# Kernel optimization log

Measured on AMD Instinct MI355X. Metric: run time of the kernel, lower is better.

The kernel has to match this reference:

```python
import jax, jax.numpy as jnp
import numpy as np

INPUT_DIM = 1024
ATTN_DIM = 512
N1 = 4096
N2 = 4096


def setup_inputs() -> dict:
    key = jax.random.key(0)
    ks = jax.random.split(key, 10)
    s_in = 1.0 / np.sqrt(INPUT_DIM)   # torch Linear default init scale
    s_at = 1.0 / np.sqrt(ATTN_DIM)
    return {
        "input1": jax.random.normal(ks[0], (N1, INPUT_DIM), jnp.float32),
        "input2": jax.random.normal(ks[1], (N2, INPUT_DIM), jnp.float32),
        "Wq": jax.random.uniform(ks[2], (INPUT_DIM, ATTN_DIM), jnp.float32, -s_in, s_in),
        "bq": jax.random.uniform(ks[3], (ATTN_DIM,), jnp.float32, -s_in, s_in),
        "Wk": jax.random.uniform(ks[4], (INPUT_DIM, ATTN_DIM), jnp.float32, -s_in, s_in),
        "bk": jax.random.uniform(ks[5], (ATTN_DIM,), jnp.float32, -s_in, s_in),
        "Wv": jax.random.uniform(ks[6], (INPUT_DIM, ATTN_DIM), jnp.float32, -s_in, s_in),
        "bv": jax.random.uniform(ks[7], (ATTN_DIM,), jnp.float32, -s_in, s_in),
        "Wo": jax.random.uniform(ks[8], (ATTN_DIM, INPUT_DIM), jnp.float32, -s_at, s_at),
        "bo": jax.random.uniform(ks[9], (INPUT_DIM,), jnp.float32, -s_at, s_at),
    }


def reference(input1, input2, Wq, bq, Wk, bk, Wv, bv, Wo, bo):
    # shared projections for both inputs
    q1 = input1 @ Wq + bq            # [N1, A]
    q2 = input2 @ Wq + bq            # [N2, A]
    k1 = input1 @ Wk + bk
    k2 = input2 @ Wk + bk
    v1 = input1 @ Wv + bv
    v2 = input2 @ Wv + bv
    # cross attention 1: input1 queries attend to input2 keys/values
    attn1 = jax.nn.softmax(q1 @ k2.T, axis=-1)   # [N1, N2]
    attn2 = jax.nn.softmax(q2 @ k1.T, axis=-1)   # [N2, N1]
    out1 = (attn1 @ v2) @ Wo + bo                # [N1, input_dim]
    out2 = (attn2 @ v1) @ Wo + bo                # [N2, input_dim]
    return (out1, out2)
```

## Files before the change

### kernel.cpp

```cpp
#include <hip/hip_runtime.h>

typedef __bf16 bf16;
typedef _Float16 f16;
typedef __bf16 bf16x8 __attribute__((ext_vector_type(8)));
typedef _Float16 f16x8 __attribute__((ext_vector_type(8)));
typedef _Float16 f16x4 __attribute__((ext_vector_type(4)));
typedef float f32x4 __attribute__((ext_vector_type(4)));
typedef unsigned int u32x4 __attribute__((ext_vector_type(4)));

#define NROWS 4096
#define DIN 1024
#define DA 512
#define NCHUNK 64

template <typename T> struct V8;
template <> struct V8<f16> { using type = f16x8; };
template <> struct V8<bf16> { using type = bf16x8; };

__device__ __forceinline__ f32x4 mfma16(f16x8 a, f16x8 b, f32x4 c) {
  return __builtin_amdgcn_mfma_f32_16x16x32_f16(a, b, c, 0, 0, 0);
}
__device__ __forceinline__ f32x4 mfma16(bf16x8 a, bf16x8 b, f32x4 c) {
  return __builtin_amdgcn_mfma_f32_16x16x32_bf16(a, b, c, 0, 0, 0);
}

__device__ __forceinline__ void gload_lds16(const void* g, void* l) {
  __builtin_amdgcn_global_load_lds((const __attribute__((address_space(1))) void*)g,
                                   (__attribute__((address_space(3))) void*)l, 16, 0, 0);
}

template <int N> __device__ __forceinline__ void vmcnt_wait() {
  if constexpr (N == 0) asm volatile("s_waitcnt vmcnt(0)" ::: "memory");
  else if constexpr (N == 1) asm volatile("s_waitcnt vmcnt(1)" ::: "memory");
  else if constexpr (N == 2) asm volatile("s_waitcnt vmcnt(2)" ::: "memory");
  else if constexpr (N == 3) asm volatile("s_waitcnt vmcnt(3)" ::: "memory");
  else if constexpr (N == 4) asm volatile("s_waitcnt vmcnt(4)" ::: "memory");
  else if constexpr (N == 5) asm volatile("s_waitcnt vmcnt(5)" ::: "memory");
  else if constexpr (N == 6) asm volatile("s_waitcnt vmcnt(6)" ::: "memory");
  else if constexpr (N == 8) asm volatile("s_waitcnt vmcnt(8)" ::: "memory");
  else static_assert(N == 0, "unsupported vmcnt");
}


__global__ void cast_kernel(const float* __restrict__ s1, const float* __restrict__ s2,
                            f16* __restrict__ d1, f16* __restrict__ d2, int n) {
  const float* s = blockIdx.z ? s2 : s1;
  f16* d = blockIdx.z ? d2 : d1;
  int i = (blockIdx.x * blockDim.x + threadIdx.x) * 4;
  if (i < n) {
    float4 v = *(const float4*)(s + i);
    f16x4 o;
    o[0] = (f16)v.x; o[1] = (f16)v.y; o[2] = (f16)v.z; o[3] = (f16)v.w;
    *(f16x4*)(d + i) = o;
  }
}

__global__ void transpose_f32(const float* __restrict__ w0, const float* __restrict__ w1,
                              const float* __restrict__ w2, f16* __restrict__ dst,
                              size_t dstride, int rows, int cols) {
  const float* s = blockIdx.z == 0 ? w0 : (blockIdx.z == 1 ? w1 : w2);
  f16* d = dst + (size_t)blockIdx.z * dstride;
  __shared__ float tile[32][33];
  int bc = blockIdx.x * 32, br = blockIdx.y * 32;
  int tx = threadIdx.x, ty = threadIdx.y;
  for (int i = ty; i < 32; i += 8)
    tile[i][tx] = s[(size_t)(br + i) * cols + bc + tx];
  __syncthreads();
  for (int i = ty; i < 32; i += 8)
    d[(size_t)(bc + i) * rows + br + tx] = (f16)tile[tx][i];
}

__global__ void rowsum_reduce(const float* __restrict__ prsP, float* __restrict__ prsT) {
  int i = blockIdx.x * 256 + threadIdx.x;
  int z = i >> 12, row = i & 4095;
  const float* p = prsP + (size_t)z * NCHUNK * NROWS + row;
  float s = 0.f;
#pragma unroll
  for (int j = 0; j < NCHUNK; ++j) s += p[(size_t)j * NROWS];
  prsT[i] = s;
}

__global__ void merge_kernel(const f16* __restrict__ pO, f16* __restrict__ mid) {
  const size_t QS = (size_t)NROWS * DA;
  size_t e = ((size_t)blockIdx.x * blockDim.x + threadIdx.x) * 8;
  int z = (int)(e / QS);
  size_t rem = e - (size_t)z * QS;
  f16x8 a = *(const f16x8*)(pO + (size_t)z * QS + rem);
  f16x8 b = *(const f16x8*)(pO + (size_t)(2 + z) * QS + rem);
  f16x8 o;
#pragma unroll
  for (int j = 0; j < 8; ++j) o[j] = (f16)((float)a[j] + (float)b[j]);
  *(f16x8*)(mid + (size_t)z * QS + rem) = o;
}


template <typename TIN>
struct G8Args {
  const TIN* A[6];
  const TIN* B[6];
  const float* bias[6];
  void* C[6];
  float* rsO[6];
  int k0[6];
  int storebf[6];
  int lda, ldb, ldc, aK;
};

template <typename TIN, int EPI, int BN, int NT, int BK = 64, int MINW = 1, int PH = 4>
__global__ __launch_bounds__(512, MINW) void g8(G8Args<TIN> args) {
  using vec8 = typename V8<TIN>::type;
  constexpr int NFR = BN / 64;
  constexpr int FPP = 8 / PH;
  constexpr int KK = BK / 32;
  constexpr int RB = BK * 2;
  constexpr int CPR = RB / 16;
  constexpr int SWM = CPR - 1;
  constexpr int SFT = (CPR == 4) ? 1 : 0;
  constexpr int ABUF = 256 * RB;
  constexpr int BBUF = BN * RB;
  constexpr int BUFSZ = ABUF + BBUF;
  constexpr int IPU = ABUF / 2 / 8192;
  __shared__ __align__(16) char smem[2 * BUFSZ];

  static_assert(PH == 4 || PH == 2, "PH in {2,4}");

  const int z = blockIdx.z;
  const TIN* __restrict__ A = args.A[z];
  const TIN* __restrict__ B = args.B[z];
  const int lda = args.lda, ldb = args.ldb, aK = args.aK;
  const int k0 = args.k0[z];

  int blkM, blkN;
  {
    const int gx = gridDim.x;
    const int nwg = gx * gridDim.y;
    const int lin = blockIdx.y * gx + blockIdx.x;
    const int q = nwg >> 3;
    const int nl = (lin & 7) * q + (lin >> 3);
    blkN = nl % gx;
    blkM = nl / gx;
  }

  const int tid = threadIdx.x;
  const int w = tid >> 6, lane = tid & 63;
  const int wm = w & 1, wn = w >> 1;
  const int lr = lane & 15, lh = lane >> 4;

  const TIN* Abase = A + (size_t)blkM * 256 * lda;
  const TIN* Bbase = B + (size_t)blkN * BN * ldb;

  f32x4 acc[8][NFR] = {};
  vec8 af[FPP][KK], bfr[NFR][KK];

#define SWZ(r_) (((r_) >> SFT) & SWM)
#define STAGE_A(buf, hf, kt)                                                    \
  {                                                                             \
    char* dst_ = smem + (buf)*BUFSZ + (hf)*(ABUF / 2);                          \
    const TIN* src_ = Abase + (size_t)((hf)*128) * lda + (size_t)(kt)*aK;       \
    _Pragma("unroll")                                                           \
    for (int i_ = 0; i_ < IPU; ++i_) {                                          \
      int c_ = i_ * 512 + tid;                                                  \
      int r_ = c_ / CPR, q_ = c_ % CPR;                                         \
      gload_lds16(src_ + (size_t)r_ * lda + ((q_ ^ SWZ(r_)) << 3),              \
                  dst_ + c_ * 16);                                              \
    }                                                                           \
  }
#define STAGE_B(buf, hf, kt)                                                    \
  {                                                                             \
    char* dst_ = smem + (buf)*BUFSZ + ABUF + (hf)*(ABUF / 2);                   \
    const TIN* src_ = Bbase + (size_t)((hf)*128) * ldb + (kt);                  \
    _Pragma("unroll")                                                           \
    for (int i_ = 0; i_ < IPU; ++i_) {                                          \
      int c_ = i_ * 512 + tid;                                                  \
      int r_ = c_ / CPR, q_ = c_ % CPR;                                         \
      gload_lds16(src_ + (size_t)r_ * ldb + ((q_ ^ SWZ(r_)) << 3),              \
                  dst_ + c_ * 16);                                              \
    }                                                                           \
  }
#define LDA_PHASE(buf, p)                                                       \
  {                                                                             \
    char* Ab_ = smem + (buf)*BUFSZ;                                             \
    _Pragma("unroll")                                                           \
    for (int fi_ = 0; fi_ < FPP; ++fi_) {                                       \
      int row_ = (((p)*FPP + fi_) * 2 + wm) * 16 + lr;                          \
      _Pragma("unroll")                                                         \
      for (int kk_ = 0; kk_ < KK; ++kk_) {                                      \
        int cc_ = (kk_ * 4 + lh) ^ SWZ(row_);                                   \
        af[fi_][kk_] = *(const vec8*)(Ab_ + row_ * RB + cc_ * 16);              \
      }                                                                         \
    }                                                                           \
  }
#define LDB_ALL(buf)                                                            \
  {                                                                             \
    char* Bb_ = smem + (buf)*BUFSZ + ABUF;                                      \
    _Pragma("unroll")                                                           \
    for (int n_ = 0; n_ < NFR; ++n_) {                                          \
      int row_ = wn * (BN / 4) + n_ * 16 + lr;                                  \
      _Pragma("unroll")                                                         \
      for (int kk_ = 0; kk_ < KK; ++kk_) {                                      \
        int cc_ = (kk_ * 4 + lh) ^ SWZ(row_);                                   \
        bfr[n_][kk_] = *(const vec8*)(Bb_ + row_ * RB + cc_ * 16);              \
      }                                                                         \
    }                                                                           \
  }
#define MFMA_PHASE(p)                                                           \
  {                                                                             \
    _Pragma("unroll")                                                           \
    for (int fi_ = 0; fi_ < FPP; ++fi_) {                                       \
      _Pragma("unroll")                                                         \
      for (int n_ = 0; n_ < NFR; ++n_) {                                        \
        _Pragma("unroll")                                                       \
        for (int kk_ = 0; kk_ < KK; ++kk_)                                      \
          acc[(p)*FPP + fi_][n_] = mfma16(af[fi_][kk_], bfr[n_][kk_],           \
                                          acc[(p)*FPP + fi_][n_]);              \
      }                                                                         \
    }                                                                           \
  }
#define BAR() __builtin_amdgcn_s_barrier()
#define LGK0()                                          \
  asm volatile("s_waitcnt lgkmcnt(0)" ::: "memory");    \
  __builtin_amdgcn_sched_barrier(0)

  if constexpr (NFR == 4) {
    STAGE_B(0, 0, k0); STAGE_B(0, 1, k0); STAGE_A(0, 0, k0); STAGE_A(0, 1, k0);
  } else {
    STAGE_B(0, 0, k0); STAGE_A(0, 0, k0); STAGE_A(0, 1, k0);
  }
  vmcnt_wait<IPU>();
  BAR();

  for (int t = 0; t < NT; ++t) {
    const int cur = t & 1, nxt = cur ^ 1;
    const int ktn = k0 + (t + 1) * BK;
    const bool st = (t < NT - 1);
    if constexpr (PH == 4) {
      if (st) { STAGE_B(nxt, 0, ktn); }
      LDB_ALL(cur);
      LDA_PHASE(cur, 0);
      BAR(); LGK0();
      __builtin_amdgcn_s_setprio(1); MFMA_PHASE(0); __builtin_amdgcn_s_setprio(0);
      BAR();
      if (st) { STAGE_B(nxt, 1, ktn); }
      LDA_PHASE(cur, 1);
      BAR(); LGK0();
      __builtin_amdgcn_s_setprio(1); MFMA_PHASE(1); __builtin_amdgcn_s_setprio(0);
      if (st) { vmcnt_wait<2 * IPU>(); }
      else    { vmcnt_wait<0>(); }
      BAR();
      if (st) { STAGE_A(nxt, 0, ktn); }
      LDA_PHASE(cur, 2);
      BAR(); LGK0();
      __builtin_amdgcn_s_setprio(1); MFMA_PHASE(2); __builtin_amdgcn_s_setprio(0);
      BAR();
      if (st) { STAGE_A(nxt, 1, ktn); }
      LDA_PHASE(cur, 3);
      BAR(); LGK0();
      __builtin_amdgcn_s_setprio(1); MFMA_PHASE(3); __builtin_amdgcn_s_setprio(0);
      if (st) { vmcnt_wait<IPU>(); }
      BAR();
    } else {
      if (st) {
        STAGE_B(nxt, 0, ktn);
        if constexpr (NFR == 4) { STAGE_B(nxt, 1, ktn); }
        STAGE_A(nxt, 0, ktn);
      }
      LDB_ALL(cur);
      LDA_PHASE(cur, 0);
      BAR(); LGK0();
      __builtin_amdgcn_s_setprio(1); MFMA_PHASE(0); __builtin_amdgcn_s_setprio(0);
      if (st) { vmcnt_wait<(NFR == 4 ? 3 : 2) * IPU>(); }
      else    { vmcnt_wait<0>(); }
      BAR();
      if (st) { STAGE_A(nxt, 1, ktn); }
      LDA_PHASE(cur, 1);
      BAR(); LGK0();
      __builtin_amdgcn_s_setprio(1); MFMA_PHASE(1); __builtin_amdgcn_s_setprio(0);
      if (st) { vmcnt_wait<IPU>(); }
      BAR();
    }
  }

  const int row0 = blkM * 256;
  const int col0 = blkN * BN + wn * (BN / 4);
  const int ldc = args.ldc;
  if constexpr (EPI == 1) {
    bf16* Pt = (bf16*)args.C[z] + (size_t)(blkN * 4 + wn) * ((size_t)NROWS * 64);
#pragma unroll
    for (int a = 0; a < 8; ++a) {
      float rsv[4] = {0.f, 0.f, 0.f, 0.f};
#pragma unroll
      for (int n = 0; n < NFR; ++n) {
#pragma unroll
        for (int rr = 0; rr < 4; ++rr) {
          int row = row0 + (a * 2 + wm) * 16 + lh * 4 + rr;
          float e = __expf(acc[a][n][rr]);
          Pt[(size_t)row * 64 + n * 16 + lr] = (bf16)e;
          rsv[rr] += e;
        }
      }
#pragma unroll
      for (int rr = 0; rr < 4; ++rr) {
        float s = rsv[rr];
        s += __shfl_xor(s, 1);
        s += __shfl_xor(s, 2);
        s += __shfl_xor(s, 4);
        s += __shfl_xor(s, 8);
        if (lr == 0) {
          int row = row0 + (a * 2 + wm) * 16 + lh * 4 + rr;
          args.rsO[z][((size_t)blkN * 4 + wn) * NROWS + row] = s;
        }
      }
    }
  } else if constexpr (EPI == 2) {
#pragma unroll
    for (int a = 0; a < 8; ++a) {
#pragma unroll
      for (int rr = 0; rr < 4; ++rr) {
        int row = row0 + (a * 2 + wm) * 16 + lh * 4 + rr;
        float rinv = 1.0f / args.rsO[z][row];
#pragma unroll
        for (int n = 0; n < NFR; ++n) {
          int col = col0 + n * 16 + lr;
          ((f16*)args.C[z])[(size_t)row * ldc + col] = (f16)(acc[a][n][rr] * rinv);
        }
      }
    }
  } else if constexpr (EPI == 0 && BN == 256) {
    if (args.storebf[z]) {
#pragma unroll
      for (int a = 0; a < 8; ++a) {
#pragma unroll
        for (int n = 0; n < NFR; ++n) {
#pragma unroll
          for (int rr = 0; rr < 4; ++rr) {
            int row_l = (a * 2 + wm) * 16 + lh * 4 + rr;
            int col_l = wn * 64 + n * 16 + lr;
            float b = acc[a][n][rr] + args.bias[z][blkN * 256 + col_l];
            int byte = col_l * 512 + (((row_l >> 3) ^ (col_l & 31)) << 4) + (row_l & 7) * 2;
            *(bf16*)(smem + byte) = (bf16)b;
          }
        }
      }
      __syncthreads();
      bf16* vt = (bf16*)args.C[z];
#pragma unroll
      for (int i = 0; i < 16; ++i) {
        int cidx = i * 512 + tid;
        int c = cidx >> 5, ch = cidx & 31;
        u32x4 v = *(const u32x4*)(smem + c * 512 + ((ch ^ (c & 31)) << 4));
        size_t dst = (size_t)(blkN * 256 + c) * NROWS + blkM * 256 + ch * 8;
        *(u32x4*)(vt + dst) = v;
      }
    } else {
#pragma unroll
      for (int a = 0; a < 8; ++a) {
#pragma unroll
        for (int n = 0; n < NFR; ++n) {
#pragma unroll
          for (int rr = 0; rr < 4; ++rr) {
            int row = row0 + (a * 2 + wm) * 16 + lh * 4 + rr;
            int col = col0 + n * 16 + lr;
            ((f16*)args.C[z])[(size_t)row * ldc + col] =
                (f16)(acc[a][n][rr] + args.bias[z][col]);
          }
        }
      }
    }
  } else {
#pragma unroll
    for (int a = 0; a < 8; ++a) {
#pragma unroll
      for (int n = 0; n < NFR; ++n) {
#pragma unroll
        for (int rr = 0; rr < 4; ++rr) {
          int row = row0 + (a * 2 + wm) * 16 + lh * 4 + rr;
          int col = col0 + n * 16 + lr;
          float v = acc[a][n][rr];
          if constexpr (EPI == 0) {
            ((f16*)args.C[z])[(size_t)row * ldc + col] = (f16)(v + args.bias[z][col]);
          } else {
            ((float*)args.C[z])[(size_t)row * ldc + col] = v + args.bias[z][col];
          }
        }
      }
    }
  }
#undef SWZ
#undef STAGE_A
#undef STAGE_B
#undef LDA_PHASE
#undef LDB_ALL
#undef MFMA_PHASE
#undef BAR
#undef LGK0
}


extern "C" void kernel_launch(void* const* d_in, const int* in_sizes, int n_in,
                              void* d_out, int out_size, void* d_ws, size_t ws_size,
                              hipStream_t stream) {
  const float* in1 = (const float*)d_in[0];
  const float* in2 = (const float*)d_in[1];
  const float* Wq = (const float*)d_in[2];
  const float* bq = (const float*)d_in[3];
  const float* Wk = (const float*)d_in[4];
  const float* bk = (const float*)d_in[5];
  const float* Wv = (const float*)d_in[6];
  const float* bv = (const float*)d_in[7];
  const float* Wo = (const float*)d_in[8];
  const float* bo = (const float*)d_in[9];
  float* out = (float*)d_out;

  const size_t IN_E = (size_t)NROWS * DIN;
  const size_t WT_E = (size_t)DA * DIN;
  const size_t QS = (size_t)NROWS * DA;
  const size_t PS = (size_t)NROWS * NROWS;

  f16* qk = (f16*)d_ws;
  f16* in_hf = qk + 4 * QS;
  bf16* vv = (bf16*)(in_hf + 2 * IN_E);
  f16* wt = (f16*)(vv + 2 * QS);
  f16* woT = wt + 3 * WT_E;
  bf16* vt = (bf16*)(woT + WT_E);
  bf16* P = vt + 2 * QS;
  f16* mid = (f16*)(P + 2 * PS);
  f16* pO = (f16*)d_ws;
  float* prsP = (float*)vv;
  float* prsT = prsP + 2 * (size_t)NCHUNK * NROWS;

  cast_kernel<<<dim3((unsigned)(IN_E / 1024), 1, 2), dim3(256), 0, stream>>>(
      in1, in2, in_hf, in_hf + IN_E, (int)IN_E);

  transpose_f32<<<dim3(DA / 32, DIN / 32, 3), dim3(32, 8), 0, stream>>>(
      Wq, Wk, Wv, wt, WT_E, DIN, DA);
  transpose_f32<<<dim3(DIN / 32, DA / 32, 1), dim3(32, 8), 0, stream>>>(
      Wo, Wo, Wo, woT, 0, DA, DIN);

  {
    G8Args<f16> a{};
    const float* bs[3] = {bq, bk, bv};
    for (int zi = 0; zi < 6; ++zi) {
      int which = (zi < 4) ? (zi & 1) : 2;
      int src = (zi < 4) ? (zi >> 1) : (zi - 4);
      a.A[zi] = in_hf + (size_t)src * IN_E;
      a.B[zi] = wt + (size_t)which * WT_E;
      a.bias[zi] = bs[which];
      a.C[zi] = (zi < 4) ? (void*)(qk + (size_t)zi * QS) : (void*)(vt + (size_t)(zi - 4) * QS);
      a.storebf[zi] = (zi >= 4);
      a.k0[zi] = 0;
    }
    a.lda = DIN; a.ldb = DIN; a.ldc = DA; a.aK = 1;
    g8<f16, 0, 256, 16, 64, 1, 2><<<dim3(2, 16, 6), dim3(512), 0, stream>>>(a);
  }

  {
    G8Args<f16> a{};
    a.A[0] = qk + 0 * QS; a.B[0] = qk + 3 * QS; a.C[0] = P;
    a.A[1] = qk + 2 * QS; a.B[1] = qk + 1 * QS; a.C[1] = P + PS;
    a.rsO[0] = prsP;
    a.rsO[1] = prsP + (size_t)NCHUNK * NROWS;
    a.k0[0] = a.k0[1] = 0;
    a.lda = DA; a.ldb = DA; a.ldc = NROWS; a.aK = 1;
    g8<f16, 1, 256, 8, 64, 1, 2><<<dim3(16, 16, 2), dim3(512), 0, stream>>>(a);
  }

  rowsum_reduce<<<dim3(32), dim3(256), 0, stream>>>(prsP, prsT);

  {
    G8Args<bf16> a{};
    for (int i = 0; i < 4; ++i) {
      int pair = i & 1, s = i >> 1;
      a.A[i] = P + (size_t)pair * PS;
      a.B[i] = vt + (size_t)(pair ^ 1) * QS;
      a.C[i] = pO + (size_t)i * QS;
      a.rsO[i] = prsT + (size_t)pair * NROWS;
      a.k0[i] = s * 2048;
      a.storebf[i] = 0;
    }
    a.lda = 64; a.ldb = NROWS; a.ldc = DA; a.aK = NROWS;
    g8<bf16, 2, 128, 32, 64, 1, 2><<<dim3(4, 16, 4), dim3(512), 0, stream>>>(a);
  }

  merge_kernel<<<dim3((unsigned)(2 * QS / 2048)), dim3(256), 0, stream>>>(pO, mid);

  {
    G8Args<f16> a{};
    a.A[0] = mid;      a.C[0] = out;
    a.A[1] = mid + QS; a.C[1] = out + (size_t)NROWS * DIN;
    a.B[0] = a.B[1] = woT;
    a.bias[0] = a.bias[1] = bo;
    a.k0[0] = a.k0[1] = 0;
    a.lda = DA; a.ldb = DA; a.ldc = DIN; a.aK = 1;
    g8<f16, 3, 128, 8, 64, 1, 2><<<dim3(8, 16, 2), dim3(512), 0, stream>>>(a);
  }
}
```

Measured before the change: 191.8 us.

## Add 4-stage BK=32 pipelined GEMM kernel for projection and score GEMMs

Measured after the change: 195.9 us. +2.1%, slower.

```diff
diff --git a/kernel.cpp b/kernel.cpp
--- a/kernel.cpp
+++ b/kernel.cpp
@@ -35,9 +35,9 @@
   else if constexpr (N == 2) asm volatile("s_waitcnt vmcnt(2)" ::: "memory");
   else if constexpr (N == 3) asm volatile("s_waitcnt vmcnt(3)" ::: "memory");
   else if constexpr (N == 4) asm volatile("s_waitcnt vmcnt(4)" ::: "memory");
-  else if constexpr (N == 5) asm volatile("s_waitcnt vmcnt(5)" ::: "memory");
   else if constexpr (N == 6) asm volatile("s_waitcnt vmcnt(6)" ::: "memory");
   else if constexpr (N == 8) asm volatile("s_waitcnt vmcnt(8)" ::: "memory");
+  else if constexpr (N == 12) asm volatile("s_waitcnt vmcnt(12)" ::: "memory");
   else static_assert(N == 0, "unsupported vmcnt");
 }
 
@@ -93,7 +93,6 @@
   *(f16x8*)(mid + (size_t)z * QS + rem) = o;
 }
 
-
 template <typename TIN>
 struct G8Args {
   const TIN* A[6];
@@ -105,6 +104,192 @@
   int storebf[6];
   int lda, ldb, ldc, aK;
 };
+
+
+template <typename TIN, int EPI, int BN, int NT>
+__global__ __launch_bounds__(512, 1) void g4d(G8Args<TIN> args) {
+  using vec8 = typename V8<TIN>::type;
+  constexpr int NFR = BN / 64;
+  constexpr int ABUF = 256 * 64;
+  constexpr int BBUF = BN * 64;
+  constexpr int TBUF = ABUF + BBUF;
+  constexpr int AR = 2, BR = BN * 4 / 512;
+  constexpr int LPT = AR + BR;
+  __shared__ __align__(16) char smem[4 * TBUF];
+  static_assert(BN == 256, "g4d tuned for BN=256");
+
+  const int z = blockIdx.z;
+  const TIN* __restrict__ A = args.A[z];
+  const TIN* __restrict__ B = args.B[z];
+  const int lda = args.lda, ldb = args.ldb, aK = args.aK;
+  const int k0 = args.k0[z];
+
+  int blkM, blkN;
+  {
+    const int gx = gridDim.x;
+    const int nwg = gx * gridDim.y;
+    const int lin = blockIdx.y * gx + blockIdx.x;
+    const int q = nwg >> 3;
+    const int nl = (lin & 7) * q + (lin >> 3);
+    blkN = nl % gx;
+    blkM = nl / gx;
+  }
+
+  const int tid = threadIdx.x;
+  const int w = tid >> 6, lane = tid & 63;
+  const int wm = w & 1, wn = w >> 1;
+  const int lr = lane & 15, lh = lane >> 4;
+
+  const TIN* Abase = A + (size_t)blkM * 256 * lda;
+  const TIN* Bbase = B + (size_t)blkN * BN * ldb;
+
+  f32x4 acc[8][NFR] = {};
+  vec8 af[8], bfr[NFR];
+
+#define STAGE4(buf, kt)                                                         \
+  {                                                                             \
+    char* da_ = smem + (buf)*TBUF;                                              \
+    const TIN* sa_ = Abase + (size_t)(kt)*aK;                                   \
+    _Pragma("unroll")                                                           \
+    for (int i_ = 0; i_ < AR; ++i_) {                                           \
+      int c_ = i_ * 512 + tid;                                                  \
+      int r_ = c_ >> 2, q_ = c_ & 3;                                            \
+      gload_lds16(sa_ + (size_t)r_ * lda + ((q_ ^ ((r_ >> 1) & 3)) << 3),       \
+                  da_ + c_ * 16);                                               \
+    }                                                                           \
+    char* db_ = smem + (buf)*TBUF + ABUF;                                       \
+    const TIN* sb_ = Bbase + (kt);                                              \
+    _Pragma("unroll")                                                           \
+    for (int i_ = 0; i_ < BR; ++i_) {                                           \
+      int c_ = i_ * 512 + tid;                                                  \
+      int r_ = c_ >> 2, q_ = c_ & 3;                                            \
+      gload_lds16(sb_ + (size_t)r_ * ldb + ((q_ ^ ((r_ >> 1) & 3)) << 3),       \
+                  db_ + c_ * 16);                                               \
+    }                                                                           \
+  }
+#define LDALL(buf)                                                              \
+  {                                                                             \
+    char* Ab_ = smem + (buf)*TBUF;                                              \
+    _Pragma("unroll")                                                           \
+    for (int a_ = 0; a_ < 8; ++a_) {                                            \
+      int row_ = (a_ * 2 + wm) * 16 + lr;                                       \
+      int cc_ = lh ^ ((row_ >> 1) & 3);                                         \
+      af[a_] = *(const vec8*)(Ab_ + row_ * 64 + cc_ * 16);                      \
+    }                                                                           \
+    char* Bb_ = smem + (buf)*TBUF + ABUF;                                       \
+    _Pragma("unroll")                                                           \
+    for (int n_ = 0; n_ < NFR; ++n_) {                                          \
+      int row_ = wn * (BN / 4) + n_ * 16 + lr;                                  \
+      int cc_ = lh ^ ((row_ >> 1) & 3);                                         \
+      bfr[n_] = *(const vec8*)(Bb_ + row_ * 64 + cc_ * 16);                     \
+    }                                                                           \
+  }
+#define BAR() __builtin_amdgcn_s_barrier()
+#define LGK0()                                          \
+  asm volatile("s_waitcnt lgkmcnt(0)" ::: "memory");    \
+  __builtin_amdgcn_sched_barrier(0)
+
+  STAGE4(0, k0); STAGE4(1, k0 + 32); STAGE4(2, k0 + 64);
+
+  for (int t = 0; t < NT; ++t) {
+    if (t + 3 < NT) { STAGE4((t + 3) & 3, k0 + (t + 3) * 32); }
+    int nf = NT - 1 - t; if (nf > 3) nf = 3;
+    if (nf == 3)      { vmcnt_wait<3 * LPT>(); }
+    else if (nf == 2) { vmcnt_wait<2 * LPT>(); }
+    else if (nf == 1) { vmcnt_wait<1 * LPT>(); }
+    else              { vmcnt_wait<0>(); }
+    BAR();
+    LDALL(t & 3);
+    LGK0();
+    __builtin_amdgcn_s_setprio(1);
+#pragma unroll
+    for (int a = 0; a < 8; ++a)
+#pragma unroll
+      for (int n = 0; n < NFR; ++n)
+        acc[a][n] = mfma16(af[a], bfr[n], acc[a][n]);
+    __builtin_amdgcn_s_setprio(0);
+    BAR();
+  }
+
+  const int row0 = blkM * 256;
+  const int col0 = blkN * BN + wn * (BN / 4);
+  const int ldc = args.ldc;
+  if constexpr (EPI == 1) {
+    bf16* Pt = (bf16*)args.C[z] + (size_t)(blkN * 4 + wn) * ((size_t)NROWS * 64);
+#pragma unroll
+    for (int a = 0; a < 8; ++a) {
+      float rsv[4] = {0.f, 0.f, 0.f, 0.f};
+#pragma unroll
+      for (int n = 0; n < NFR; ++n) {
+#pragma unroll
+        for (int rr = 0; rr < 4; ++rr) {
+          int row = row0 + (a * 2 + wm) * 16 + lh * 4 + rr;
+          float e = __expf(acc[a][n][rr]);
+          Pt[(size_t)row * 64 + n * 16 + lr] = (bf16)e;
+          rsv[rr] += e;
+        }
+      }
+#pragma unroll
+      for (int rr = 0; rr < 4; ++rr) {
+        float s = rsv[rr];
+        s += __shfl_xor(s, 1);
+        s += __shfl_xor(s, 2);
+        s += __shfl_xor(s, 4);
+        s += __shfl_xor(s, 8);
+        if (lr == 0) {
+          int row = row0 + (a * 2 + wm) * 16 + lh * 4 + rr;
+          args.rsO[z][((size_t)blkN * 4 + wn) * NROWS + row] = s;
+        }
+      }
+    }
+  } else {
+    if (args.storebf[z]) {
+#pragma unroll
+      for (int a = 0; a < 8; ++a) {
+#pragma unroll
+        for (int n = 0; n < NFR; ++n) {
+#pragma unroll
+          for (int rr = 0; rr < 4; ++rr) {
+            int row_l = (a * 2 + wm) * 16 + lh * 4 + rr;
+            int col_l = wn * 64 + n * 16 + lr;
+            float b = acc[a][n][rr] + args.bias[z][blkN * 256 + col_l];
+            int byte = col_l * 512 + (((row_l >> 3) ^ (col_l & 31)) << 4) + (row_l & 7) * 2;
+            *(bf16*)(smem + byte) = (bf16)b;
+          }
+        }
+      }
+      __syncthreads();
+      bf16* vt = (bf16*)args.C[z];
+#pragma unroll
+      for (int i = 0; i < 16; ++i) {
+        int cidx = i * 512 + tid;
+        int c = cidx >> 5, ch = cidx & 31;
+        u32x4 v = *(const u32x4*)(smem + c * 512 + ((ch ^ (c & 31)) << 4));
+        size_t dst = (size_t)(blkN * 256 + c) * NROWS + blkM * 256 + ch * 8;
+        *(u32x4*)(vt + dst) = v;
+      }
+    } else {
+#pragma unroll
+      for (int a = 0; a < 8; ++a) {
+#pragma unroll
+        for (int n = 0; n < NFR; ++n) {
+#pragma unroll
+          for (int rr = 0; rr < 4; ++rr) {
+            int row = row0 + (a * 2 + wm) * 16 + lh * 4 + rr;
+            int col = col0 + n * 16 + lr;
+            ((f16*)args.C[z])[(size_t)row * ldc + col] =
+                (f16)(acc[a][n][rr] + args.bias[z][col]);
+          }
+        }
+      }
+    }
+  }
+#undef STAGE4
+#undef LDALL
+#undef BAR
+#undef LGK0
+}
+
 
 template <typename TIN, int EPI, int BN, int NT, int BK = 64, int MINW = 1, int PH = 4>
 __global__ __launch_bounds__(512, MINW) void g8(G8Args<TIN> args) {
@@ -283,35 +468,7 @@
   const int row0 = blkM * 256;
   const int col0 = blkN * BN + wn * (BN / 4);
   const int ldc = args.ldc;
-  if constexpr (EPI == 1) {
-    bf16* Pt = (bf16*)args.C[z] + (size_t)(blkN * 4 + wn) * ((size_t)NROWS * 64);
-#pragma unroll
-    for (int a = 0; a < 8; ++a) {
-      float rsv[4] = {0.f, 0.f, 0.f, 0.f};
-#pragma unroll
-      for (int n = 0; n < NFR; ++n) {
-#pragma unroll
-        for (int rr = 0; rr < 4; ++rr) {
-          int row = row0 + (a * 2 + wm) * 16 + lh * 4 + rr;
-          float e = __expf(acc[a][n][rr]);
-          Pt[(size_t)row * 64 + n * 16 + lr] = (bf16)e;
-          rsv[rr] += e;
-        }
-      }
-#pragma unroll
-      for (int rr = 0; rr < 4; ++rr) {
-        float s = rsv[rr];
-        s += __shfl_xor(s, 1);
-        s += __shfl_xor(s, 2);
-        s += __shfl_xor(s, 4);
-        s += __shfl_xor(s, 8);
-        if (lr == 0) {
-          int row = row0 + (a * 2 + wm) * 16 + lh * 4 + rr;
-          args.rsO[z][((size_t)blkN * 4 + wn) * NROWS + row] = s;
-        }
-      }
-    }
-  } else if constexpr (EPI == 2) {
+  if constexpr (EPI == 2) {
 #pragma unroll
     for (int a = 0; a < 8; ++a) {
 #pragma unroll
@@ -325,47 +482,6 @@
         }
       }
     }
-  } else if constexpr (EPI == 0 && BN == 256) {
-    if (args.storebf[z]) {
-#pragma unroll
-      for (int a = 0; a < 8; ++a) {
-#pragma unroll
-        for (int n = 0; n < NFR; ++n) {
-#pragma unroll
-          for (int rr = 0; rr < 4; ++rr) {
-            int row_l = (a * 2 + wm) * 16 + lh * 4 + rr;
-            int col_l = wn * 64 + n * 16 + lr;
-            float b = acc[a][n][rr] + args.bias[z][blkN * 256 + col_l];
-            int byte = col_l * 512 + (((row_l >> 3) ^ (col_l & 31)) << 4) + (row_l & 7) * 2;
-            *(bf16*)(smem + byte) = (bf16)b;
-          }
-        }
-      }
-      __syncthreads();
-      bf16* vt = (bf16*)args.C[z];
-#pragma unroll
-      for (int i = 0; i < 16; ++i) {
-        int cidx = i * 512 + tid;
-        int c = cidx >> 5, ch = cidx & 31;
-        u32x4 v = *(const u32x4*)(smem + c * 512 + ((ch ^ (c & 31)) << 4));
-        size_t dst = (size_t)(blkN * 256 + c) * NROWS + blkM * 256 + ch * 8;
-        *(u32x4*)(vt + dst) = v;
-      }
-    } else {
-#pragma unroll
-      for (int a = 0; a < 8; ++a) {
-#pragma unroll
-        for (int n = 0; n < NFR; ++n) {
-#pragma unroll
-          for (int rr = 0; rr < 4; ++rr) {
-            int row = row0 + (a * 2 + wm) * 16 + lh * 4 + rr;
-            int col = col0 + n * 16 + lr;
-            ((f16*)args.C[z])[(size_t)row * ldc + col] =
-                (f16)(acc[a][n][rr] + args.bias[z][col]);
-          }
-        }
-      }
-    }
   } else {
 #pragma unroll
     for (int a = 0; a < 8; ++a) {
@@ -375,12 +491,7 @@
         for (int rr = 0; rr < 4; ++rr) {
           int row = row0 + (a * 2 + wm) * 16 + lh * 4 + rr;
           int col = col0 + n * 16 + lr;
-          float v = acc[a][n][rr];
-          if constexpr (EPI == 0) {
-            ((f16*)args.C[z])[(size_t)row * ldc + col] = (f16)(v + args.bias[z][col]);
-          } else {
-            ((float*)args.C[z])[(size_t)row * ldc + col] = v + args.bias[z][col];
-          }
+          ((float*)args.C[z])[(size_t)row * ldc + col] = acc[a][n][rr] + args.bias[z][col];
         }
       }
     }
@@ -450,7 +561,7 @@
       a.k0[zi] = 0;
     }
     a.lda = DIN; a.ldb = DIN; a.ldc = DA; a.aK = 1;
-    g8<f16, 0, 256, 16, 64, 1, 2><<<dim3(2, 16, 6), dim3(512), 0, stream>>>(a);
+    g4d<f16, 0, 256, 32><<<dim3(2, 16, 6), dim3(512), 0, stream>>>(a);
   }
 
   {
@@ -461,7 +572,7 @@
     a.rsO[1] = prsP + (size_t)NCHUNK * NROWS;
     a.k0[0] = a.k0[1] = 0;
     a.lda = DA; a.ldb = DA; a.ldc = NROWS; a.aK = 1;
-    g8<f16, 1, 256, 8, 64, 1, 2><<<dim3(16, 16, 2), dim3(512), 0, stream>>>(a);
+    g4d<f16, 1, 256, 16><<<dim3(16, 16, 2), dim3(512), 0, stream>>>(a);
   }
 
   rowsum_reduce<<<dim3(32), dim3(256), 0, stream>>>(prsP, prsT);
```

## Replace QK^T score GEMM with dedicated 128x128 tile kernel

Applied to the files above, without the earlier changes.

Result: slower. 205.6 us (+7.2%).

```diff
diff --git a/kernel.cpp b/kernel.cpp
--- a/kernel.cpp
+++ b/kernel.cpp
@@ -35,7 +35,6 @@
   else if constexpr (N == 2) asm volatile("s_waitcnt vmcnt(2)" ::: "memory");
   else if constexpr (N == 3) asm volatile("s_waitcnt vmcnt(3)" ::: "memory");
   else if constexpr (N == 4) asm volatile("s_waitcnt vmcnt(4)" ::: "memory");
-  else if constexpr (N == 5) asm volatile("s_waitcnt vmcnt(5)" ::: "memory");
   else if constexpr (N == 6) asm volatile("s_waitcnt vmcnt(6)" ::: "memory");
   else if constexpr (N == 8) asm volatile("s_waitcnt vmcnt(8)" ::: "memory");
   else static_assert(N == 0, "unsupported vmcnt");
@@ -91,6 +90,113 @@
 #pragma unroll
   for (int j = 0; j < 8; ++j) o[j] = (f16)((float)a[j] + (float)b[j]);
   *(f16x8*)(mid + (size_t)z * QS + rem) = o;
+}
+
+
+__global__ __launch_bounds__(256, 4) void qk128(
+    const f16* __restrict__ q1, const f16* __restrict__ k2,
+    const f16* __restrict__ q2, const f16* __restrict__ k1,
+    bf16* __restrict__ Pout, float* __restrict__ prsP) {
+  __shared__ __align__(16) f16 As[128 * 64];
+  __shared__ __align__(16) f16 Bs[128 * 64];
+  const int z = blockIdx.z;
+  const f16* __restrict__ A = z ? q2 : q1;
+  const f16* __restrict__ B = z ? k1 : k2;
+  bf16* __restrict__ Pz = Pout + (size_t)z * ((size_t)NROWS * NROWS);
+  float* __restrict__ rsO = prsP + (size_t)z * NCHUNK * NROWS;
+
+  int blkM, blkN;
+  {
+    const int lin = blockIdx.y * 32 + blockIdx.x;
+    const int nl = (lin & 7) * 128 + (lin >> 3);
+    blkN = nl & 31;
+    blkM = nl >> 5;
+  }
+
+  const int tid = threadIdx.x;
+  const int w = tid >> 6, lane = tid & 63;
+  const int wr = w >> 1, wc = w & 1;
+  const int lr = lane & 15, lh = lane >> 4;
+
+  const f16* Abase = A + (size_t)blkM * 128 * DA;
+  const f16* Bbase = B + (size_t)blkN * 128 * DA;
+
+  f32x4 acc[4][4] = {};
+
+  for (int kt = 0; kt < DA; kt += 64) {
+#pragma unroll
+    for (int i = 0; i < 4; ++i) {
+      int c = i * 256 + tid;
+      int r = c >> 3, q = c & 7;
+      gload_lds16(Abase + (size_t)r * DA + kt + ((q ^ (r & 7)) << 3),
+                  (char*)As + c * 16);
+    }
+#pragma unroll
+    for (int i = 0; i < 4; ++i) {
+      int c = i * 256 + tid;
+      int r = c >> 3, q = c & 7;
+      gload_lds16(Bbase + (size_t)r * DA + kt + ((q ^ (r & 7)) << 3),
+                  (char*)Bs + c * 16);
+    }
+    __syncthreads();
+
+    f16x8 af[4][2], bfr[4][2];
+#pragma unroll
+    for (int m = 0; m < 4; ++m)
+#pragma unroll
+      for (int kk = 0; kk < 2; ++kk) {
+        int row = wr * 64 + m * 16 + lr;
+        int cc = (kk * 4 + lh) ^ (row & 7);
+        af[m][kk] = *(const f16x8*)((char*)As + row * 128 + cc * 16);
+      }
+#pragma unroll
+    for (int n = 0; n < 4; ++n)
+#pragma unroll
+      for (int kk = 0; kk < 2; ++kk) {
+        int row = wc * 64 + n * 16 + lr;
+        int cc = (kk * 4 + lh) ^ (row & 7);
+        bfr[n][kk] = *(const f16x8*)((char*)Bs + row * 128 + cc * 16);
+      }
+
+#pragma unroll
+    for (int m = 0; m < 4; ++m)
+#pragma unroll
+      for (int n = 0; n < 4; ++n)
+#pragma unroll
+        for (int kk = 0; kk < 2; ++kk)
+          acc[m][n] = mfma16(af[m][kk], bfr[n][kk], acc[m][n]);
+    __syncthreads();
+  }
+
+  const int kc = blkN * 2 + wc;
+  bf16* Pt = Pz + (size_t)kc * ((size_t)NROWS * 64);
+  const int row0 = blkM * 128 + wr * 64;
+#pragma unroll
+  for (int m = 0; m < 4; ++m) {
+    float rsv[4] = {0.f, 0.f, 0.f, 0.f};
+#pragma unroll
+    for (int n = 0; n < 4; ++n) {
+#pragma unroll
+      for (int rr = 0; rr < 4; ++rr) {
+        int row = row0 + m * 16 + lh * 4 + rr;
+        float e = __expf(acc[m][n][rr]);
+        Pt[(size_t)row * 64 + n * 16 + lr] = (bf16)e;
+        rsv[rr] += e;
+      }
+    }
+#pragma unroll
+    for (int rr = 0; rr < 4; ++rr) {
+      float s = rsv[rr];
+      s += __shfl_xor(s, 1);
+      s += __shfl_xor(s, 2);
+      s += __shfl_xor(s, 4);
+      s += __shfl_xor(s, 8);
+      if (lr == 0) {
+        int row = row0 + m * 16 + lh * 4 + rr;
+        rsO[(size_t)kc * NROWS + row] = s;
+      }
+    }
+  }
 }
 
 
@@ -283,35 +389,7 @@
   const int row0 = blkM * 256;
   const int col0 = blkN * BN + wn * (BN / 4);
   const int ldc = args.ldc;
-  if constexpr (EPI == 1) {
-    bf16* Pt = (bf16*)args.C[z] + (size_t)(blkN * 4 + wn) * ((size_t)NROWS * 64);
-#pragma unroll
-    for (int a = 0; a < 8; ++a) {
-      float rsv[4] = {0.f, 0.f, 0.f, 0.f};
-#pragma unroll
-      for (int n = 0; n < NFR; ++n) {
-#pragma unroll
-        for (int rr = 0; rr < 4; ++rr) {
-          int row = row0 + (a * 2 + wm) * 16 + lh * 4 + rr;
-          float e = __expf(acc[a][n][rr]);
-          Pt[(size_t)row * 64 + n * 16 + lr] = (bf16)e;
-          rsv[rr] += e;
-        }
-      }
-#pragma unroll
-      for (int rr = 0; rr < 4; ++rr) {
-        float s = rsv[rr];
-        s += __shfl_xor(s, 1);
-        s += __shfl_xor(s, 2);
-        s += __shfl_xor(s, 4);
-        s += __shfl_xor(s, 8);
-        if (lr == 0) {
-          int row = row0 + (a * 2 + wm) * 16 + lh * 4 + rr;
-          args.rsO[z][((size_t)blkN * 4 + wn) * NROWS + row] = s;
-        }
-      }
-    }
-  } else if constexpr (EPI == 2) {
+  if constexpr (EPI == 2) {
 #pragma unroll
     for (int a = 0; a < 8; ++a) {
 #pragma unroll
@@ -453,16 +531,8 @@
     g8<f16, 0, 256, 16, 64, 1, 2><<<dim3(2, 16, 6), dim3(512), 0, stream>>>(a);
   }
 
-  {
-    G8Args<f16> a{};
-    a.A[0] = qk + 0 * QS; a.B[0] = qk + 3 * QS; a.C[0] = P;
-    a.A[1] = qk + 2 * QS; a.B[1] = qk + 1 * QS; a.C[1] = P + PS;
-    a.rsO[0] = prsP;
-    a.rsO[1] = prsP + (size_t)NCHUNK * NROWS;
-    a.k0[0] = a.k0[1] = 0;
-    a.lda = DA; a.ldb = DA; a.ldc = NROWS; a.aK = 1;
-    g8<f16, 1, 256, 8, 64, 1, 2><<<dim3(16, 16, 2), dim3(512), 0, stream>>>(a);
-  }
+  qk128<<<dim3(32, 32, 2), dim3(256), 0, stream>>>(
+      qk + 0 * QS, qk + 3 * QS, qk + 2 * QS, qk + 1 * QS, P, prsP);
 
   rowsum_reduce<<<dim3(32), dim3(256), 0, stream>>>(prsP, prsT);
 
```

## Fuse split-K partial merge into output projection GEMM

Applied to the files above, without the earlier changes.

After: 188.7 us. Within noise of the previous version (-1.6%).

```diff
diff --git a/kernel.cpp b/kernel.cpp
--- a/kernel.cpp
+++ b/kernel.cpp
@@ -35,7 +35,6 @@
   else if constexpr (N == 2) asm volatile("s_waitcnt vmcnt(2)" ::: "memory");
   else if constexpr (N == 3) asm volatile("s_waitcnt vmcnt(3)" ::: "memory");
   else if constexpr (N == 4) asm volatile("s_waitcnt vmcnt(4)" ::: "memory");
-  else if constexpr (N == 5) asm volatile("s_waitcnt vmcnt(5)" ::: "memory");
   else if constexpr (N == 6) asm volatile("s_waitcnt vmcnt(6)" ::: "memory");
   else if constexpr (N == 8) asm volatile("s_waitcnt vmcnt(8)" ::: "memory");
   else static_assert(N == 0, "unsupported vmcnt");
@@ -80,17 +79,97 @@
   prsT[i] = s;
 }
 
-__global__ void merge_kernel(const f16* __restrict__ pO, f16* __restrict__ mid) {
+
+__global__ __launch_bounds__(512) void out_fused(const f16* __restrict__ pO,
+                                                 const f16* __restrict__ woT,
+                                                 const float* __restrict__ bo,
+                                                 float* __restrict__ out) {
+  __shared__ __align__(16) f16 As[128 * 64];
+  __shared__ __align__(16) f16 Bs[128 * 64];
+  const int z = blockIdx.z;
   const size_t QS = (size_t)NROWS * DA;
-  size_t e = ((size_t)blockIdx.x * blockDim.x + threadIdx.x) * 8;
-  int z = (int)(e / QS);
-  size_t rem = e - (size_t)z * QS;
-  f16x8 a = *(const f16x8*)(pO + (size_t)z * QS + rem);
-  f16x8 b = *(const f16x8*)(pO + (size_t)(2 + z) * QS + rem);
-  f16x8 o;
-#pragma unroll
-  for (int j = 0; j < 8; ++j) o[j] = (f16)((float)a[j] + (float)b[j]);
-  *(f16x8*)(mid + (size_t)z * QS + rem) = o;
+  const f16* __restrict__ A0 = pO + (size_t)z * QS;
+  const f16* __restrict__ A1 = pO + (size_t)(2 + z) * QS;
+  float* __restrict__ Cg = out + (size_t)z * NROWS * DIN;
+
+  int blkM, blkN;
+  {
+    const int gx = gridDim.x;
+    const int nwg = gx * gridDim.y;
+    const int lin = blockIdx.y * gx + blockIdx.x;
+    const int q = nwg >> 3;
+    const int nl = (lin & 7) * q + (lin >> 3);
+    blkN = nl % gx;
+    blkM = nl / gx;
+  }
+
+  const int tid = threadIdx.x;
+  const int w = tid >> 6, lane = tid & 63;
+  const int wr = w >> 2, wc = w & 3;
+  const int lrow = lane & 15, lhi = lane >> 4;
+
+  const size_t abase = (size_t)blkM * 128 * DA;
+  const f16* Bbase = woT + (size_t)blkN * 128 * DA;
+
+  f32x4 acc[4][2] = {};
+
+  for (int kt = 0; kt < DA; kt += 64) {
+#pragma unroll
+    for (int it = 0; it < 2; ++it) {
+      int cidx = (it * 8 + w) * 64 + lane;
+      int row = cidx >> 3;
+      int col = (cidx & 7) << 3;
+      size_t off = abase + (size_t)row * DA + kt + col;
+      f16x8 a = *(const f16x8*)(A0 + off);
+      f16x8 b = *(const f16x8*)(A1 + off);
+      f16x8 s;
+#pragma unroll
+      for (int j = 0; j < 8; ++j) s[j] = (f16)((float)a[j] + (float)b[j]);
+      *(f16x8*)((char*)As + (size_t)cidx * 16) = s;
+    }
+#pragma unroll
+    for (int it = 0; it < 2; ++it) {
+      int cidx = (it * 8 + w) * 64 + lane;
+      int row = cidx >> 3;
+      int col = (cidx & 7) << 3;
+      gload_lds16(Bbase + (size_t)row * DA + kt + col, (char*)Bs + (size_t)cidx * 16);
+    }
+    __syncthreads();
+
+    f16x8 af[4][2], bfr[2][2];
+#pragma unroll
+    for (int m = 0; m < 4; ++m)
+#pragma unroll
+      for (int kk = 0; kk < 2; ++kk)
+        af[m][kk] = *(const f16x8*)&As[(wr * 64 + m * 16 + lrow) * 64 + kk * 32 + lhi * 8];
+#pragma unroll
+    for (int n = 0; n < 2; ++n)
+#pragma unroll
+      for (int kk = 0; kk < 2; ++kk)
+        bfr[n][kk] = *(const f16x8*)&Bs[(wc * 32 + n * 16 + lrow) * 64 + kk * 32 + lhi * 8];
+
+#pragma unroll
+    for (int m = 0; m < 4; ++m)
+#pragma unroll
+      for (int n = 0; n < 2; ++n)
+#pragma unroll
+        for (int kk = 0; kk < 2; ++kk)
+          acc[m][n] = mfma16(af[m][kk], bfr[n][kk], acc[m][n]);
+    __syncthreads();
+  }
+
+  const int row0 = blkM * 128 + wr * 64;
+  const int col0 = blkN * 128 + wc * 32;
+#pragma unroll
+  for (int m = 0; m < 4; ++m)
+#pragma unroll
+    for (int n = 0; n < 2; ++n)
+#pragma unroll
+      for (int r = 0; r < 4; ++r) {
+        int row = row0 + m * 16 + lhi * 4 + r;
+        int col = col0 + n * 16 + lrow;
+        Cg[(size_t)row * DIN + col] = acc[m][n][r] + bo[col];
+      }
 }
 
 
@@ -423,7 +502,6 @@
   f16* woT = wt + 3 * WT_E;
   bf16* vt = (bf16*)(woT + WT_E);
   bf16* P = vt + 2 * QS;
-  f16* mid = (f16*)(P + 2 * PS);
   f16* pO = (f16*)d_ws;
   float* prsP = (float*)vv;
   float* prsT = prsP + 2 * (size_t)NCHUNK * NROWS;
@@ -481,16 +559,6 @@
     g8<bf16, 2, 128, 32, 64, 1, 2><<<dim3(4, 16, 4), dim3(512), 0, stream>>>(a);
   }
 
-  merge_kernel<<<dim3((unsigned)(2 * QS / 2048)), dim3(256), 0, stream>>>(pO, mid);
-
-  {
-    G8Args<f16> a{};
-    a.A[0] = mid;      a.C[0] = out;
-    a.A[1] = mid + QS; a.C[1] = out + (size_t)NROWS * DIN;
-    a.B[0] = a.B[1] = woT;
-    a.bias[0] = a.bias[1] = bo;
-    a.k0[0] = a.k0[1] = 0;
-    a.lda = DA; a.ldb = DA; a.ldc = DIN; a.aK = 1;
-    g8<f16, 3, 128, 8, 64, 1, 2><<<dim3(8, 16, 2), dim3(512), 0, stream>>>(a);
-  }
-}
+  out_fused<<<dim3(DIN / 128, NROWS / 128, 2), dim3(512), 0, stream>>>(
+      pO, woT, bo, out);
+}
```
